# Optimization experiments

Measured on AMD Instinct MI355X. Metric: run time of the kernel, lower is better.

## Reference

```python
import jax, jax.numpy as jnp
import numpy as np

N_JOINTS = 50
N_BONES = 50
# getSkeletalModelStructure() stand-in: 50 bones over 50 joints (i -> (i+1) % 50)
SRC = jnp.arange(N_BONES)
DST = (jnp.arange(N_BONES) + 1) % N_JOINTS
EPS = 1e-8


def _length_direct(x):
    # x: [B, T, 150] -> lengths [B, T, 50], directions [B, T, 150]
    B, T, _ = x.shape
    joints = x.reshape(B, T, N_JOINTS, 3)
    diff = joints[:, :, SRC, :] - joints[:, :, DST, :]      # [B, T, 50, 3]
    length = jnp.sqrt(jnp.sum(diff * diff, axis=-1))        # [B, T, 50]
    direct = diff / (length[..., None] + EPS)               # [B, T, 50, 3]
    return length, direct.reshape(B, T, N_BONES * 3)


def setup_inputs() -> dict:
    key = jax.random.key(0)
    k1, k2 = jax.random.split(key)
    preds = jax.random.normal(k1, (128, 1024, 150), dtype=jnp.float32)
    targets = jax.random.normal(k2, (128, 1024, 150), dtype=jnp.float32)
    return {"preds": preds, "targets": targets}


def reference(preds, targets):
    target_pad = 0.0
    loss_mask = (targets != target_pad).astype(jnp.float32)
    preds_masked = preds * loss_mask
    targets_masked = targets * loss_mask
    _, pd = _length_direct(preds_masked)
    _, td = _length_direct(targets_masked)
    pd = pd * loss_mask[:, :, :150]
    td = td * loss_mask[:, :, :150]
    # criterion = L1 (mean), criterion_bone = MSE (mean); loss_scale = 1.0
    loss = jnp.mean(jnp.abs(preds_masked - targets_masked)) + 0.1 * jnp.mean((pd - td) ** 2)
    return loss
```

## Files before the change

kernel.cpp:

```cpp
#include <hip/hip_runtime.h>


#define ROW_F    150
#define ROWS_PW  4
#define SPAN_F   (ROWS_PW * ROW_F)
#define SPAN_F4  (SPAN_F / 4)
#define WAVES_PB 4
#define GRID     2048
#define TOTAL_WAVES (GRID * WAVES_PB)

__global__ __launch_bounds__(256, 8) void loss_kernel(
    const float* __restrict__ preds,
    const float* __restrict__ targets,
    float* __restrict__ out,
    int iters, float inv_count)
{
    const float EPS = 1e-8f;
    __shared__ float sp[WAVES_PB][SPAN_F];
    __shared__ float st[WAVES_PB][SPAN_F];
    __shared__ float wsum[WAVES_PB];

    const int tid  = threadIdx.x;
    const int lane = tid & 63;
    const int wid  = tid >> 6;

    const float4* gp4 = reinterpret_cast<const float4*>(preds);
    const float4* gt4 = reinterpret_cast<const float4*>(targets);
    float4* sp4 = reinterpret_cast<float4*>(sp[wid]);
    float4* st4 = reinterpret_cast<float4*>(st[wid]);

    const int g0 = lane, g1 = lane + 64, g2 = lane + 128;
    const bool w2 = (g2 < SPAN_F4);
    const int g2c = w2 ? g2 : (SPAN_F4 - 1);

    const int row = lane >> 4;
    const int seg = lane & 15;
    const int j0 = (seg < 2) ? seg * 4 : 8 + (seg - 2) * 3;
    const int j1 = j0 + ((seg < 2) ? 4 : 3);

    float l1 = 0.0f, mse = 0.0f;

    const int wglobal = blockIdx.x * WAVES_PB + wid;

    size_t sb = (size_t)wglobal * SPAN_F4;
    float4 rp0 = gp4[sb + g0], rp1 = gp4[sb + g1], rp2 = gp4[sb + g2c];
    float4 rt0 = gt4[sb + g0], rt1 = gt4[sb + g1], rt2 = gt4[sb + g2c];

    for (int it = 0; it < iters; ++it) {
        sp4[g0] = rp0; st4[g0] = rt0;
        sp4[g1] = rp1; st4[g1] = rt1;
        if (w2) { sp4[g2] = rp2; st4[g2] = rt2; }

        if (it + 1 < iters) {
            size_t nb = (size_t)(wglobal + (size_t)(it + 1) * TOTAL_WAVES) * SPAN_F4;
            rp0 = gp4[nb + g0]; rp1 = gp4[nb + g1]; rp2 = gp4[nb + g2c];
            rt0 = gt4[nb + g0]; rt1 = gt4[nb + g1]; rt2 = gt4[nb + g2c];
        }

        const float* rpb = &sp[wid][row * ROW_F];
        const float* rtb = &st[wid][row * ROW_F];

        float pmP[3], tmP[3];
#pragma unroll
        for (int c = 0; c < 3; ++c) {
            float t = rtb[3 * j0 + c];
            float p = rpb[3 * j0 + c];
            pmP[c] = (t != 0.0f) ? p : 0.0f;
            tmP[c] = t;
            l1 += fabsf(pmP[c] - tmP[c]);
        }

        for (int b = j0; b < j1; ++b) {
            int jn = b + 1;
            if (jn == 50) jn = 0;
            float pmN[3], tmN[3];
#pragma unroll
            for (int c = 0; c < 3; ++c) {
                float t = rtb[3 * jn + c];
                float p = rpb[3 * jn + c];
                pmN[c] = (t != 0.0f) ? p : 0.0f;
                tmN[c] = t;
            }
            if (jn < j1 && jn != 0) {
#pragma unroll
                for (int c = 0; c < 3; ++c) l1 += fabsf(pmN[c] - tmN[c]);
            }
            float dp[3], dt[3], lp = 0.0f, lt = 0.0f;
#pragma unroll
            for (int c = 0; c < 3; ++c) {
                dp[c] = pmP[c] - pmN[c];
                dt[c] = tmP[c] - tmN[c];
                lp += dp[c] * dp[c];
                lt += dt[c] * dt[c];
            }
            float ip = __builtin_amdgcn_rcpf(__builtin_amdgcn_sqrtf(lp) + EPS);
            float iq = __builtin_amdgcn_rcpf(__builtin_amdgcn_sqrtf(lt) + EPS);
#pragma unroll
            for (int c = 0; c < 3; ++c) {
                float d = dp[c] * ip - dt[c] * iq;
                d = (tmP[c] != 0.0f) ? d : 0.0f;
                mse += d * d;
            }
#pragma unroll
            for (int c = 0; c < 3; ++c) { pmP[c] = pmN[c]; tmP[c] = tmN[c]; }
        }
    }

    float part = (l1 + 0.1f * mse) * inv_count;
#pragma unroll
    for (int off = 32; off > 0; off >>= 1)
        part += __shfl_down(part, off, 64);

    if (lane == 0) wsum[wid] = part;
    __syncthreads();
    if (tid == 0) {
        atomicAdd(out, wsum[0] + wsum[1] + wsum[2] + wsum[3]);
    }
}

extern "C" void kernel_launch(void* const* d_in, const int* in_sizes, int n_in,
                              void* d_out, int out_size, void* d_ws, size_t ws_size,
                              hipStream_t stream)
{
    const float* preds   = (const float*)d_in[0];
    const float* targets = (const float*)d_in[1];
    float* out = (float*)d_out;

    hipMemsetAsync(out, 0, sizeof(float) * out_size, stream);

    int n_elems = in_sizes[0];
    int n_rows  = n_elems / ROW_F;
    int spans   = n_rows / ROWS_PW;
    float inv_count = 1.0f / (float)n_elems;

    int iters = spans / TOTAL_WAVES;
    loss_kernel<<<GRID, 256, 0, stream>>>(preds, targets, out, iters, inv_count);
}
```

Baseline: 179.1 us.

## Map one row per wave with lane-per-joint and shuffle neighbor exchange

Replaces LDS staging of four-row spans with a layout where each lane loads one joint's three coordinates of a single row and fetches the adjacent joint via a wave shuffle. This removes shared-memory writes/reads and the uneven per-lane bone loop. In exchange, 14 of 64 lanes idle, loads become scalar dwords instead of float4, and fewer bytes are in flight per wave per iteration, which may reduce bandwidth on a memory-bound kernel.

```diff
diff --git a/kernel.cpp b/kernel.cpp
--- a/kernel.cpp
+++ b/kernel.cpp
@@ -2,11 +2,9 @@
 
 
 #define ROW_F    150
-#define ROWS_PW  4
-#define SPAN_F   (ROWS_PW * ROW_F)
-#define SPAN_F4  (SPAN_F / 4)
+#define N_JOINT  50
+#define GRID     2048
 #define WAVES_PB 4
-#define GRID     2048
 #define TOTAL_WAVES (GRID * WAVES_PB)
 
 __global__ __launch_bounds__(256, 8) void loss_kernel(
@@ -16,94 +14,66 @@
     int iters, float inv_count)
 {
     const float EPS = 1e-8f;
-    __shared__ float sp[WAVES_PB][SPAN_F];
-    __shared__ float st[WAVES_PB][SPAN_F];
     __shared__ float wsum[WAVES_PB];
 
     const int tid  = threadIdx.x;
     const int lane = tid & 63;
     const int wid  = tid >> 6;
-
-    const float4* gp4 = reinterpret_cast<const float4*>(preds);
-    const float4* gt4 = reinterpret_cast<const float4*>(targets);
-    float4* sp4 = reinterpret_cast<float4*>(sp[wid]);
-    float4* st4 = reinterpret_cast<float4*>(st[wid]);
-
-    const int g0 = lane, g1 = lane + 64, g2 = lane + 128;
-    const bool w2 = (g2 < SPAN_F4);
-    const int g2c = w2 ? g2 : (SPAN_F4 - 1);
-
-    const int row = lane >> 4;
-    const int seg = lane & 15;
-    const int j0 = (seg < 2) ? seg * 4 : 8 + (seg - 2) * 3;
-    const int j1 = j0 + ((seg < 2) ? 4 : 3);
-
-    float l1 = 0.0f, mse = 0.0f;
+    const bool act = (lane < N_JOINT);
+    const int  sel = (lane + 1 == N_JOINT) ? 0 : lane + 1;
 
     const int wglobal = blockIdx.x * WAVES_PB + wid;
+    const ptrdiff_t STRIDE = (ptrdiff_t)TOTAL_WAVES * ROW_F;
 
-    size_t sb = (size_t)wglobal * SPAN_F4;
-    float4 rp0 = gp4[sb + g0], rp1 = gp4[sb + g1], rp2 = gp4[sb + g2c];
-    float4 rt0 = gt4[sb + g0], rt1 = gt4[sb + g1], rt2 = gt4[sb + g2c];
+    const int eoff = act ? 3 * lane : 0;
+
+    const float* pp = preds   + (size_t)wglobal * ROW_F + eoff;
+    const float* tp = targets + (size_t)wglobal * ROW_F + eoff;
+
+    float l1 = 0.f, mse = 0.f;
+
+    float cp0 = pp[0], cp1 = pp[1], cp2 = pp[2];
+    float ct0 = tp[0], ct1 = tp[1], ct2 = tp[2];
+    pp += STRIDE; tp += STRIDE;
 
     for (int it = 0; it < iters; ++it) {
-        sp4[g0] = rp0; st4[g0] = rt0;
-        sp4[g1] = rp1; st4[g1] = rt1;
-        if (w2) { sp4[g2] = rp2; st4[g2] = rt2; }
-
+        float np0 = 0.f, np1 = 0.f, np2 = 0.f, nt0 = 0.f, nt1 = 0.f, nt2 = 0.f;
         if (it + 1 < iters) {
-            size_t nb = (size_t)(wglobal + (size_t)(it + 1) * TOTAL_WAVES) * SPAN_F4;
-            rp0 = gp4[nb + g0]; rp1 = gp4[nb + g1]; rp2 = gp4[nb + g2c];
-            rt0 = gt4[nb + g0]; rt1 = gt4[nb + g1]; rt2 = gt4[nb + g2c];
+            np0 = pp[0]; np1 = pp[1]; np2 = pp[2];
+            nt0 = tp[0]; nt1 = tp[1]; nt2 = tp[2];
+            pp += STRIDE; tp += STRIDE;
         }
 
-        const float* rpb = &sp[wid][row * ROW_F];
-        const float* rtb = &st[wid][row * ROW_F];
+        float tm0 = act ? ct0 : 0.f;
+        float tm1 = act ? ct1 : 0.f;
+        float tm2 = act ? ct2 : 0.f;
+        float pm0 = (tm0 != 0.f) ? cp0 : 0.f;
+        float pm1 = (tm1 != 0.f) ? cp1 : 0.f;
+        float pm2 = (tm2 != 0.f) ? cp2 : 0.f;
 
-        float pmP[3], tmP[3];
-#pragma unroll
-        for (int c = 0; c < 3; ++c) {
-            float t = rtb[3 * j0 + c];
-            float p = rpb[3 * j0 + c];
-            pmP[c] = (t != 0.0f) ? p : 0.0f;
-            tmP[c] = t;
-            l1 += fabsf(pmP[c] - tmP[c]);
-        }
+        l1 += fabsf(pm0 - tm0) + fabsf(pm1 - tm1) + fabsf(pm2 - tm2);
 
-        for (int b = j0; b < j1; ++b) {
-            int jn = b + 1;
-            if (jn == 50) jn = 0;
-            float pmN[3], tmN[3];
-#pragma unroll
-            for (int c = 0; c < 3; ++c) {
-                float t = rtb[3 * jn + c];
-                float p = rpb[3 * jn + c];
-                pmN[c] = (t != 0.0f) ? p : 0.0f;
-                tmN[c] = t;
-            }
-            if (jn < j1 && jn != 0) {
-#pragma unroll
-                for (int c = 0; c < 3; ++c) l1 += fabsf(pmN[c] - tmN[c]);
-            }
-            float dp[3], dt[3], lp = 0.0f, lt = 0.0f;
-#pragma unroll
-            for (int c = 0; c < 3; ++c) {
-                dp[c] = pmP[c] - pmN[c];
-                dt[c] = tmP[c] - tmN[c];
-                lp += dp[c] * dp[c];
-                lt += dt[c] * dt[c];
-            }
-            float ip = __builtin_amdgcn_rcpf(__builtin_amdgcn_sqrtf(lp) + EPS);
-            float iq = __builtin_amdgcn_rcpf(__builtin_amdgcn_sqrtf(lt) + EPS);
-#pragma unroll
-            for (int c = 0; c < 3; ++c) {
-                float d = dp[c] * ip - dt[c] * iq;
-                d = (tmP[c] != 0.0f) ? d : 0.0f;
-                mse += d * d;
-            }
-#pragma unroll
-            for (int c = 0; c < 3; ++c) { pmP[c] = pmN[c]; tmP[c] = tmN[c]; }
-        }
+        float pn0 = __shfl(pm0, sel, 64);
+        float pn1 = __shfl(pm1, sel, 64);
+        float pn2 = __shfl(pm2, sel, 64);
+        float tn0 = __shfl(tm0, sel, 64);
+        float tn1 = __shfl(tm1, sel, 64);
+        float tn2 = __shfl(tm2, sel, 64);
+
+        float dp0 = pm0 - pn0, dp1 = pm1 - pn1, dp2 = pm2 - pn2;
+        float dt0 = tm0 - tn0, dt1 = tm1 - tn1, dt2 = tm2 - tn2;
+        float lp = dp0 * dp0 + dp1 * dp1 + dp2 * dp2;
+        float lt = dt0 * dt0 + dt1 * dt1 + dt2 * dt2;
+        float ip = __builtin_amdgcn_rcpf(__builtin_amdgcn_sqrtf(lp) + EPS);
+        float iq = __builtin_amdgcn_rcpf(__builtin_amdgcn_sqrtf(lt) + EPS);
+
+        float d0 = dp0 * ip - dt0 * iq; d0 = (tm0 != 0.f) ? d0 : 0.f;
+        float d1 = dp1 * ip - dt1 * iq; d1 = (tm1 != 0.f) ? d1 : 0.f;
+        float d2 = dp2 * ip - dt2 * iq; d2 = (tm2 != 0.f) ? d2 : 0.f;
+        mse += d0 * d0 + d1 * d1 + d2 * d2;
+
+        cp0 = np0; cp1 = np1; cp2 = np2;
+        ct0 = nt0; ct1 = nt1; ct2 = nt2;
     }
 
     float part = (l1 + 0.1f * mse) * inv_count;
@@ -130,9 +100,8 @@
 
     int n_elems = in_sizes[0];
     int n_rows  = n_elems / ROW_F;
-    int spans   = n_rows / ROWS_PW;
     float inv_count = 1.0f / (float)n_elems;
 
-    int iters = spans / TOTAL_WAVES;
+    int iters = n_rows / TOTAL_WAVES;
     loss_kernel<<<GRID, 256, 0, stream>>>(preds, targets, out, iters, inv_count);
 }
```

After: 187.0 us. +4.4%, slower.
